# Optimization experiments

Measured on AMD Instinct MI355X. Metric: run time of the kernel, lower is better.

## Reference

```python
import jax, jax.numpy as jnp
import numpy as np

B, C, C2, E = 4, 1024, 1024, 1024
D = 1024          # context_size (d_q = d_kv)
NH = 16           # module's n_heads arg -> actual head_dim after the quirky view
G = D // NH       # effective number of head groups = 64


def setup_inputs() -> dict:
    key = jax.random.key(0)
    ks = jax.random.split(key, 6)
    s = 0.02
    return {
        "x1": jax.random.normal(ks[0], (B, C, E), dtype=jnp.float32),
        "x2": jax.random.normal(ks[1], (B, C2, E), dtype=jnp.float32),
        "W_q": jax.random.normal(ks[2], (E, D), dtype=jnp.float32) * s,
        "W_k": jax.random.normal(ks[3], (E, D), dtype=jnp.float32) * s,
        "W_v": jax.random.normal(ks[4], (E, D), dtype=jnp.float32) * s,
        "W_o": jax.random.normal(ks[5], (D, D), dtype=jnp.float32) * s,
    }


def _split_heads(t):
    # (B, S, D) -> view (B, S, G, NH) -> transpose(1,2) -> (B, G, S, NH)
    b, s, _ = t.shape
    return jnp.transpose(t.reshape(b, s, G, NH), (0, 2, 1, 3))


def reference(x1, x2, W_q, W_k, W_v, W_o):
    Q = _split_heads(x1 @ W_q)   # (B, G, C, NH)
    K = _split_heads(x2 @ W_k)   # (B, G, C2, NH)
    V = _split_heads(x2 @ W_v)   # (B, G, C2, NH)
    scale = 1.0 / jnp.sqrt(jnp.asarray(NH, dtype=Q.dtype))
    scores = jnp.einsum("bgqh,bgkh->bgqk", Q, K) * scale  # (B, G, C, C2)
    w = jax.nn.softmax(scores, axis=-1)
    out = jnp.einsum("bgqk,bgkh->bgqh", w, V)             # (B, G, C, NH)
    out = jnp.transpose(out, (0, 2, 1, 3)).reshape(B, C, D)
    return out @ W_o  # dropout p=0 -> identity
```

## Files before the change

### kernel.cpp

```cpp
#include <hip/hip_runtime.h>


typedef _Float16 f16x8 __attribute__((ext_vector_type(8)));
typedef _Float16 f16x4 __attribute__((ext_vector_type(4)));
typedef _Float16 f16x2 __attribute__((ext_vector_type(2)));
typedef float    f32x4 __attribute__((ext_vector_type(4)));

#define GLOAD_LDS16(gp, lp)                                              \
    __builtin_amdgcn_global_load_lds(                                    \
        (const __attribute__((address_space(1))) void*)(gp),             \
        (__attribute__((address_space(3))) void*)(lp), 16, 0, 0)

static __device__ __forceinline__ f16x8 pack8(f32x4 p0, f32x4 p1) {
    f16x2 a = __builtin_bit_cast(f16x2, __builtin_amdgcn_cvt_pkrtz(p0[0], p0[1]));
    f16x2 b = __builtin_bit_cast(f16x2, __builtin_amdgcn_cvt_pkrtz(p0[2], p0[3]));
    f16x2 c = __builtin_bit_cast(f16x2, __builtin_amdgcn_cvt_pkrtz(p1[0], p1[1]));
    f16x2 d = __builtin_bit_cast(f16x2, __builtin_amdgcn_cvt_pkrtz(p1[2], p1[3]));
    f16x8 r;
    r[0] = a[0]; r[1] = a[1]; r[2] = b[0]; r[3] = b[1];
    r[4] = c[0]; r[5] = c[1]; r[6] = d[0]; r[7] = d[1];
    return r;
}

__global__ __launch_bounds__(256) void cvt2_kernel(const float* __restrict__ x1,
                                                   const float* __restrict__ x2,
                                                   _Float16* __restrict__ y1,
                                                   _Float16* __restrict__ y2) {
    int i = blockIdx.x * 256 + threadIdx.x;
    const float* x = (i < 1048576) ? x1 : x2;
    _Float16* y = (i < 1048576) ? y1 : y2;
    int j = i & 1048575;
    float4 v = ((const float4*)x)[j];
    f16x4 h = { (_Float16)v.x, (_Float16)v.y, (_Float16)v.z, (_Float16)v.w };
    ((f16x4*)y)[j] = h;
}

__global__ __launch_bounds__(256) void transpose_cvt4_kernel(
        const float* __restrict__ W0, const float* __restrict__ W1,
        const float* __restrict__ W2, const float* __restrict__ W3,
        _Float16* __restrict__ T0, _Float16* __restrict__ T1,
        _Float16* __restrict__ T2, _Float16* __restrict__ T3) {
    int z = blockIdx.z;
    const float* W = (z == 0) ? W0 : (z == 1) ? W1 : (z == 2) ? W2 : W3;
    _Float16* WT = (z == 0) ? T0 : (z == 1) ? T1 : (z == 2) ? T2 : T3;
    __shared__ float tile[32][33];
    int tx = threadIdx.x, ty = threadIdx.y;
    int c0 = blockIdx.x * 32, r0 = blockIdx.y * 32;
#pragma unroll
    for (int i = 0; i < 32; i += 8)
        tile[ty + i][tx] = W[(r0 + ty + i) * 1024 + (c0 + tx)];
    __syncthreads();
#pragma unroll
    for (int i = 0; i < 32; i += 8)
        WT[(c0 + ty + i) * 1024 + (r0 + tx)] = (_Float16)tile[tx][ty + i];
}

template <bool OUTF32>
static __device__ __forceinline__ void gemm_body(const _Float16* __restrict__ A,
                                                 const _Float16* __restrict__ BT,
                                                 void* __restrict__ Cout,
                                                 _Float16* As, _Float16* Bs) {
    const int tid = threadIdx.x, lane = tid & 63, wave = tid >> 6;
    const int wm = wave >> 1, wn = wave & 1;
    const int col = lane & 15, quad = lane >> 4;
    const int m0 = blockIdx.y * 128, n0 = blockIdx.x * 128;

    f32x4 acc[4][4];
#pragma unroll
    for (int i = 0; i < 4; i++)
#pragma unroll
        for (int j = 0; j < 4; j++) acc[i][j] = (f32x4){0.f, 0.f, 0.f, 0.f};

    const int srow = wave * 8 + (lane >> 3);
    const int sch = (lane & 7) * 8;
    const _Float16* Ag = A + (size_t)(m0 + srow) * 1024 + sch;
    const _Float16* Bg = BT + (size_t)(n0 + srow) * 1024 + sch;
    _Float16* Asl = As + wave * 512;
    _Float16* Bsl = Bs + wave * 512;

    for (int kt = 0; kt < 16; kt++) {
        __syncthreads();
#pragma unroll
        for (int c = 0; c < 4; c++) {
            GLOAD_LDS16(Ag + (size_t)(c * 32) * 1024 + kt * 64, Asl + c * 2048);
            GLOAD_LDS16(Bg + (size_t)(c * 32) * 1024 + kt * 64, Bsl + c * 2048);
        }
        __syncthreads();
#pragma unroll
        for (int ki = 0; ki < 2; ki++) {
            f16x8 af[4], bf[4];
#pragma unroll
            for (int i = 0; i < 4; i++)
                af[i] = *(const f16x8*)(As + (wm * 64 + i * 16 + col) * 64 + ki * 32 + quad * 8);
#pragma unroll
            for (int j = 0; j < 4; j++)
                bf[j] = *(const f16x8*)(Bs + (wn * 64 + j * 16 + col) * 64 + ki * 32 + quad * 8);
#pragma unroll
            for (int i = 0; i < 4; i++)
#pragma unroll
                for (int j = 0; j < 4; j++)
                    acc[i][j] = __builtin_amdgcn_mfma_f32_16x16x32_f16(af[i], bf[j], acc[i][j], 0, 0, 0);
        }
    }

#pragma unroll
    for (int i = 0; i < 4; i++)
#pragma unroll
        for (int ii = 0; ii < 4; ii++) {
            int row = m0 + wm * 64 + i * 16 + quad * 4 + ii;
#pragma unroll
            for (int j = 0; j < 4; j++) {
                int cc = n0 + wn * 64 + j * 16 + col;
                if (OUTF32) ((float*)Cout)[(size_t)row * 1024 + cc] = acc[i][j][ii];
                else ((_Float16*)Cout)[(size_t)row * 1024 + cc] = (_Float16)acc[i][j][ii];
            }
        }
}

__global__ __launch_bounds__(256, 3) void gemm_qkv_kernel(
        const _Float16* __restrict__ x1h, const _Float16* __restrict__ x2h,
        const _Float16* __restrict__ WqT, const _Float16* __restrict__ WkT,
        const _Float16* __restrict__ WvT,
        _Float16* __restrict__ Qh, _Float16* __restrict__ Kh, _Float16* __restrict__ Vh) {
    __shared__ _Float16 As[128 * 64], Bs[128 * 64];
    int z = blockIdx.z;
    const _Float16* A = (z == 0) ? x1h : x2h;
    const _Float16* BT = (z == 0) ? WqT : (z == 1) ? WkT : WvT;
    _Float16* C = (z == 0) ? Qh : (z == 1) ? Kh : Vh;
    gemm_body<false>(A, BT, (void*)C, As, Bs);
}

__global__ __launch_bounds__(256, 3) void gemm_wo_kernel(const _Float16* __restrict__ Ah,
                                                         const _Float16* __restrict__ WoT,
                                                         float* __restrict__ out) {
    __shared__ _Float16 As[128 * 64], Bs[128 * 64];
    gemm_body<true>(Ah, WoT, (void*)out, As, Bs);
}

__global__ __launch_bounds__(512, 8) void attn_kernel(const _Float16* __restrict__ Qh,
                                                      const _Float16* __restrict__ Kh,
                                                      const _Float16* __restrict__ Vh,
                                                      _Float16* __restrict__ Ah) {
    int pair = blockIdx.y;
    int b = pair >> 6, g = pair & 63;
    __shared__ _Float16 Ks[512 * 16];
    __shared__ _Float16 Vts[16 * 512];

    const _Float16* Kg = Kh + (size_t)(b * 1024) * 1024 + g * 16;
    const _Float16* Vg = Vh + (size_t)(b * 1024) * 1024 + g * 16;
    int tid = threadIdx.x;
    int lane = tid & 63, wave = tid >> 6;
    int col = lane & 15, quad = lane >> 4;
    int q0 = blockIdx.x * 256 + wave * 32;

    f16x4 qf[2];
    const _Float16* qb = Qh + (size_t)(b * 1024 + q0 + col) * 1024 + g * 16 + quad * 4;
#pragma unroll
    for (int qg = 0; qg < 2; qg++) {
        f16x4 t = *(const f16x4*)(qb + (size_t)qg * 16 * 1024);
#pragma unroll
        for (int j = 0; j < 4; j++) qf[qg][j] = (_Float16)((float)t[j] * 0.360673760f);
    }

    f32x4 O[2], L[2];
#pragma unroll
    for (int qg = 0; qg < 2; qg++) {
        O[qg] = (f32x4){0.f, 0.f, 0.f, 0.f};
        L[qg] = (f32x4){0.f, 0.f, 0.f, 0.f};
    }
    f16x8 ones8;
#pragma unroll
    for (int j = 0; j < 8; j++) ones8[j] = (_Float16)1.f;
    const f32x4 zero = {0.f, 0.f, 0.f, 0.f};
    const int krow0 = (col >> 2) * 8 + (col & 3);
    const int vrot = 72 * col;

    for (int c = 0; c < 2; c++) {
        if (c) __syncthreads();
#pragma unroll
        for (int it = 0; it < 2; it++) {
            int row = it * 256 + (tid >> 1);
            int part = (tid & 1) * 8;
            *(uint4*)(Ks + row * 16 + part) =
                *(const uint4*)(Kg + (size_t)(c * 512 + row) * 1024 + part);
        }
#pragma unroll
        for (int it = 0; it < 2; it++) {
            int row = it * 256 + (tid >> 1);
            int part = (tid & 1) * 8;
            f16x8 v = *(const f16x8*)(Vg + (size_t)(c * 512 + row) * 1024 + part);
#pragma unroll
            for (int j = 0; j < 8; j++) {
                int h = part + j;
                Vts[h * 512 + ((row + 72 * h) & 511)] = v[j];
            }
        }
        __syncthreads();

#pragma unroll 4
        for (int t = 0; t < 16; t++) {
            const _Float16* kb = Ks + (t * 32 + krow0) * 16 + quad * 4;
            f16x4 ak0 = *(const f16x4*)(kb);
            f16x4 ak1 = *(const f16x4*)(kb + 4 * 16);
            f16x8 av = *(const f16x8*)(Vts + col * 512 + ((t * 32 + quad * 8 + vrot) & 511));
#pragma unroll
            for (int qg = 0; qg < 2; qg++) {
                f32x4 s0 = __builtin_amdgcn_mfma_f32_16x16x16f16(ak0, qf[qg], zero, 0, 0, 0);
                f32x4 s1 = __builtin_amdgcn_mfma_f32_16x16x16f16(ak1, qf[qg], zero, 0, 0, 0);
                f32x4 p0, p1;
#pragma unroll
                for (int i = 0; i < 4; i++) p0[i] = __builtin_amdgcn_exp2f(s0[i]);
#pragma unroll
                for (int i = 0; i < 4; i++) p1[i] = __builtin_amdgcn_exp2f(s1[i]);
                f16x8 pb = pack8(p0, p1);
                O[qg] = __builtin_amdgcn_mfma_f32_16x16x32_f16(av, pb, O[qg], 0, 0, 0);
                L[qg] = __builtin_amdgcn_mfma_f32_16x16x32_f16(ones8, pb, L[qg], 0, 0, 0);
            }
        }
    }

    _Float16* ob = Ah + (size_t)(b * 1024 + q0 + col) * 1024 + g * 16 + quad * 4;
#pragma unroll
    for (int qg = 0; qg < 2; qg++) {
        float rl = 1.0f / L[qg][0];
        f16x4 ov;
#pragma unroll
        for (int i = 0; i < 4; i++) ov[i] = (_Float16)(O[qg][i] * rl);
        *(f16x4*)(ob + (size_t)qg * 16 * 1024) = ov;
    }
}

extern "C" void kernel_launch(void* const* d_in, const int* in_sizes, int n_in,
                              void* d_out, int out_size, void* d_ws, size_t ws_size,
                              hipStream_t stream) {
    const float* x1 = (const float*)d_in[0];
    const float* x2 = (const float*)d_in[1];
    const float* Wq = (const float*)d_in[2];
    const float* Wk = (const float*)d_in[3];
    const float* Wv = (const float*)d_in[4];
    const float* Wo = (const float*)d_in[5];

    char* ws = (char*)d_ws;
    const size_t MB = 1u << 20;
    if (ws_size < 56 * MB) return;

    _Float16* x1h = (_Float16*)(ws + 0 * MB);
    _Float16* x2h = (_Float16*)(ws + 8 * MB);
    _Float16* WqT = (_Float16*)(ws + 16 * MB);
    _Float16* WkT = (_Float16*)(ws + 18 * MB);
    _Float16* WvT = (_Float16*)(ws + 20 * MB);
    _Float16* WoT = (_Float16*)(ws + 22 * MB);
    _Float16* Qh  = (_Float16*)(ws + 24 * MB);
    _Float16* Kh  = (_Float16*)(ws + 32 * MB);
    _Float16* Vh  = (_Float16*)(ws + 40 * MB);
    _Float16* Ah  = (_Float16*)(ws + 48 * MB);

    cvt2_kernel<<<8192, 256, 0, stream>>>(x1, x2, x1h, x2h);

    transpose_cvt4_kernel<<<dim3(32, 32, 4), dim3(32, 8), 0, stream>>>(
        Wq, Wk, Wv, Wo, WqT, WkT, WvT, WoT);

    gemm_qkv_kernel<<<dim3(8, 32, 3), 256, 0, stream>>>(x1h, x2h, WqT, WkT, WvT, Qh, Kh, Vh);

    attn_kernel<<<dim3(4, 256), 512, 0, stream>>>(Qh, Kh, Vh, Ah);

    gemm_wo_kernel<<<dim3(8, 32), 256, 0, stream>>>(Ah, WoT, (float*)d_out);
}
```

Before: 210.4 us.

## Switch attention to 32x32x16 MFMA with fused row-sum and merge prep kernels

The attention inner loop now uses 32x32x16 MFMA instructions for both the score and PV products. Lanes 16-31 of the B operand read a shared vector of ones, so the softmax denominator lands in the same accumulator and the separate L MFMA is gone. K and V are stored in shared memory with new permuted layouts that match the larger MFMA operand shapes. The input conversion and weight transpose kernels are also merged into one launch, removing one kernel's launch overhead. The risks are higher register pressure from the 16-wide accumulator and possible bank conflicts in the new LDS layouts.

```diff
diff --git a/kernel.cpp b/kernel.cpp
--- a/kernel.cpp
+++ b/kernel.cpp
@@ -5,54 +5,56 @@
 typedef _Float16 f16x4 __attribute__((ext_vector_type(4)));
 typedef _Float16 f16x2 __attribute__((ext_vector_type(2)));
 typedef float    f32x4 __attribute__((ext_vector_type(4)));
+typedef float    f32x16 __attribute__((ext_vector_type(16)));
 
 #define GLOAD_LDS16(gp, lp)                                              \
     __builtin_amdgcn_global_load_lds(                                    \
         (const __attribute__((address_space(1))) void*)(gp),             \
         (__attribute__((address_space(3))) void*)(lp), 16, 0, 0)
 
-static __device__ __forceinline__ f16x8 pack8(f32x4 p0, f32x4 p1) {
-    f16x2 a = __builtin_bit_cast(f16x2, __builtin_amdgcn_cvt_pkrtz(p0[0], p0[1]));
-    f16x2 b = __builtin_bit_cast(f16x2, __builtin_amdgcn_cvt_pkrtz(p0[2], p0[3]));
-    f16x2 c = __builtin_bit_cast(f16x2, __builtin_amdgcn_cvt_pkrtz(p1[0], p1[1]));
-    f16x2 d = __builtin_bit_cast(f16x2, __builtin_amdgcn_cvt_pkrtz(p1[2], p1[3]));
+static __device__ __forceinline__ f16x8 pack8f(const float* p) {
+    f16x2 a = __builtin_bit_cast(f16x2, __builtin_amdgcn_cvt_pkrtz(p[0], p[1]));
+    f16x2 b = __builtin_bit_cast(f16x2, __builtin_amdgcn_cvt_pkrtz(p[2], p[3]));
+    f16x2 c = __builtin_bit_cast(f16x2, __builtin_amdgcn_cvt_pkrtz(p[4], p[5]));
+    f16x2 d = __builtin_bit_cast(f16x2, __builtin_amdgcn_cvt_pkrtz(p[6], p[7]));
     f16x8 r;
     r[0] = a[0]; r[1] = a[1]; r[2] = b[0]; r[3] = b[1];
     r[4] = c[0]; r[5] = c[1]; r[6] = d[0]; r[7] = d[1];
     return r;
 }
 
-__global__ __launch_bounds__(256) void cvt2_kernel(const float* __restrict__ x1,
-                                                   const float* __restrict__ x2,
-                                                   _Float16* __restrict__ y1,
-                                                   _Float16* __restrict__ y2) {
-    int i = blockIdx.x * 256 + threadIdx.x;
-    const float* x = (i < 1048576) ? x1 : x2;
-    _Float16* y = (i < 1048576) ? y1 : y2;
-    int j = i & 1048575;
-    float4 v = ((const float4*)x)[j];
-    f16x4 h = { (_Float16)v.x, (_Float16)v.y, (_Float16)v.z, (_Float16)v.w };
-    ((f16x4*)y)[j] = h;
-}
-
-__global__ __launch_bounds__(256) void transpose_cvt4_kernel(
+__global__ __launch_bounds__(256) void prep_kernel(
+        const float* __restrict__ x1, const float* __restrict__ x2,
         const float* __restrict__ W0, const float* __restrict__ W1,
         const float* __restrict__ W2, const float* __restrict__ W3,
+        _Float16* __restrict__ y1, _Float16* __restrict__ y2,
         _Float16* __restrict__ T0, _Float16* __restrict__ T1,
         _Float16* __restrict__ T2, _Float16* __restrict__ T3) {
-    int z = blockIdx.z;
-    const float* W = (z == 0) ? W0 : (z == 1) ? W1 : (z == 2) ? W2 : W3;
-    _Float16* WT = (z == 0) ? T0 : (z == 1) ? T1 : (z == 2) ? T2 : T3;
-    __shared__ float tile[32][33];
-    int tx = threadIdx.x, ty = threadIdx.y;
-    int c0 = blockIdx.x * 32, r0 = blockIdx.y * 32;
-#pragma unroll
-    for (int i = 0; i < 32; i += 8)
-        tile[ty + i][tx] = W[(r0 + ty + i) * 1024 + (c0 + tx)];
-    __syncthreads();
-#pragma unroll
-    for (int i = 0; i < 32; i += 8)
-        WT[(c0 + ty + i) * 1024 + (r0 + tx)] = (_Float16)tile[tx][ty + i];
+    int bx = blockIdx.x, tid = threadIdx.x;
+    if (bx < 8192) {
+        int i = bx * 256 + tid;
+        const float* x = (i < 1048576) ? x1 : x2;
+        _Float16* y = (i < 1048576) ? y1 : y2;
+        int j = i & 1048575;
+        float4 v = ((const float4*)x)[j];
+        f16x4 h = { (_Float16)v.x, (_Float16)v.y, (_Float16)v.z, (_Float16)v.w };
+        ((f16x4*)y)[j] = h;
+    } else {
+        int z = (bx - 8192) >> 10;
+        const float* W = (z == 0) ? W0 : (z == 1) ? W1 : (z == 2) ? W2 : W3;
+        _Float16* WT = (z == 0) ? T0 : (z == 1) ? T1 : (z == 2) ? T2 : T3;
+        int t = (bx - 8192) & 1023;
+        int c0 = (t & 31) * 32, r0 = (t >> 5) * 32;
+        __shared__ float tile[32][33];
+        int tx = tid & 31, ty = tid >> 5;
+#pragma unroll
+        for (int i = 0; i < 32; i += 8)
+            tile[ty + i][tx] = W[(r0 + ty + i) * 1024 + (c0 + tx)];
+        __syncthreads();
+#pragma unroll
+        for (int i = 0; i < 32; i += 8)
+            WT[(c0 + ty + i) * 1024 + (r0 + tx)] = (_Float16)tile[tx][ty + i];
+    }
 }
 
 template <bool OUTF32>
@@ -143,91 +145,78 @@
                                                       _Float16* __restrict__ Ah) {
     int pair = blockIdx.y;
     int b = pair >> 6, g = pair & 63;
-    __shared__ _Float16 Ks[512 * 16];
-    __shared__ _Float16 Vts[16 * 512];
+    __shared__ _Float16 KA[8192];
+    __shared__ _Float16 VA[8192];
+    __shared__ _Float16 ones[8];
 
     const _Float16* Kg = Kh + (size_t)(b * 1024) * 1024 + g * 16;
     const _Float16* Vg = Vh + (size_t)(b * 1024) * 1024 + g * 16;
     int tid = threadIdx.x;
+    if (tid < 8) ones[tid] = (_Float16)1.f;
+
     int lane = tid & 63, wave = tid >> 6;
-    int col = lane & 15, quad = lane >> 4;
+    int n = lane & 31, h5 = lane >> 5;
     int q0 = blockIdx.x * 256 + wave * 32;
 
-    f16x4 qf[2];
-    const _Float16* qb = Qh + (size_t)(b * 1024 + q0 + col) * 1024 + g * 16 + quad * 4;
-#pragma unroll
-    for (int qg = 0; qg < 2; qg++) {
-        f16x4 t = *(const f16x4*)(qb + (size_t)qg * 16 * 1024);
-#pragma unroll
-        for (int j = 0; j < 4; j++) qf[qg][j] = (_Float16)((float)t[j] * 0.360673760f);
-    }
-
-    f32x4 O[2], L[2];
-#pragma unroll
-    for (int qg = 0; qg < 2; qg++) {
-        O[qg] = (f32x4){0.f, 0.f, 0.f, 0.f};
-        L[qg] = (f32x4){0.f, 0.f, 0.f, 0.f};
-    }
-    f16x8 ones8;
-#pragma unroll
-    for (int j = 0; j < 8; j++) ones8[j] = (_Float16)1.f;
-    const f32x4 zero = {0.f, 0.f, 0.f, 0.f};
-    const int krow0 = (col >> 2) * 8 + (col & 3);
-    const int vrot = 72 * col;
+    f16x8 qf;
+    {
+        f16x8 t = *(const f16x8*)(Qh + (size_t)(b * 1024 + q0 + n) * 1024 + g * 16 + h5 * 8);
+#pragma unroll
+        for (int j = 0; j < 8; j++) qf[j] = (_Float16)((float)t[j] * 0.360673760f);
+    }
+
+    f32x16 acc = {0.f, 0.f, 0.f, 0.f, 0.f, 0.f, 0.f, 0.f,
+                  0.f, 0.f, 0.f, 0.f, 0.f, 0.f, 0.f, 0.f};
+    const f32x16 zero16 = acc;
+    const _Float16* vbase = (n < 16) ? (VA + (n + 16 * h5) * 8) : ones;
+    const int vstep = (n < 16) ? 256 : 0;
 
     for (int c = 0; c < 2; c++) {
         if (c) __syncthreads();
 #pragma unroll
         for (int it = 0; it < 2; it++) {
             int row = it * 256 + (tid >> 1);
-            int part = (tid & 1) * 8;
-            *(uint4*)(Ks + row * 16 + part) =
-                *(const uint4*)(Kg + (size_t)(c * 512 + row) * 1024 + part);
+            int part = tid & 1;
+            int pm = (row & 19) | ((row & 4) << 1) | ((row & 8) >> 1);
+            *(uint4*)(KA + (((row >> 5) * 64) + pm + 32 * part) * 8) =
+                *(const uint4*)(Kg + (size_t)(c * 512 + row) * 1024 + part * 8);
         }
 #pragma unroll
         for (int it = 0; it < 2; it++) {
             int row = it * 256 + (tid >> 1);
-            int part = (tid & 1) * 8;
-            f16x8 v = *(const f16x8*)(Vg + (size_t)(c * 512 + row) * 1024 + part);
-#pragma unroll
-            for (int j = 0; j < 8; j++) {
-                int h = part + j;
-                Vts[h * 512 + ((row + 72 * h) & 511)] = v[j];
-            }
-        }
-        __syncthreads();
-
-#pragma unroll 4
+            int part = tid & 1;
+            f16x8 v = *(const f16x8*)(Vg + (size_t)(c * 512 + row) * 1024 + part * 8);
+            int base = (row >> 4) * 256 + ((row >> 3) & 1) * 128 + part * 64 + (row & 7);
+#pragma unroll
+            for (int j = 0; j < 8; j++) VA[base + j * 8] = v[j];
+        }
+        __syncthreads();
+
+#pragma unroll 2
         for (int t = 0; t < 16; t++) {
-            const _Float16* kb = Ks + (t * 32 + krow0) * 16 + quad * 4;
-            f16x4 ak0 = *(const f16x4*)(kb);
-            f16x4 ak1 = *(const f16x4*)(kb + 4 * 16);
-            f16x8 av = *(const f16x8*)(Vts + col * 512 + ((t * 32 + quad * 8 + vrot) & 511));
-#pragma unroll
-            for (int qg = 0; qg < 2; qg++) {
-                f32x4 s0 = __builtin_amdgcn_mfma_f32_16x16x16f16(ak0, qf[qg], zero, 0, 0, 0);
-                f32x4 s1 = __builtin_amdgcn_mfma_f32_16x16x16f16(ak1, qf[qg], zero, 0, 0, 0);
-                f32x4 p0, p1;
-#pragma unroll
-                for (int i = 0; i < 4; i++) p0[i] = __builtin_amdgcn_exp2f(s0[i]);
-#pragma unroll
-                for (int i = 0; i < 4; i++) p1[i] = __builtin_amdgcn_exp2f(s1[i]);
-                f16x8 pb = pack8(p0, p1);
-                O[qg] = __builtin_amdgcn_mfma_f32_16x16x32_f16(av, pb, O[qg], 0, 0, 0);
-                L[qg] = __builtin_amdgcn_mfma_f32_16x16x32_f16(ones8, pb, L[qg], 0, 0, 0);
-            }
-        }
-    }
-
-    _Float16* ob = Ah + (size_t)(b * 1024 + q0 + col) * 1024 + g * 16 + quad * 4;
-#pragma unroll
-    for (int qg = 0; qg < 2; qg++) {
-        float rl = 1.0f / L[qg][0];
-        f16x4 ov;
-#pragma unroll
-        for (int i = 0; i < 4; i++) ov[i] = (_Float16)(O[qg][i] * rl);
-        *(f16x4*)(ob + (size_t)qg * 16 * 1024) = ov;
-    }
+            f16x8 ak = *(const f16x8*)(KA + (t * 64 + lane) * 8);
+            f32x16 s = __builtin_amdgcn_mfma_f32_32x32x16_f16(ak, qf, zero16, 0, 0, 0);
+            float p[16];
+#pragma unroll
+            for (int i = 0; i < 16; i++) p[i] = __builtin_amdgcn_exp2f(s[i]);
+            f16x8 pb0 = pack8f(p);
+            f16x8 pb1 = pack8f(p + 8);
+            f16x8 av0 = *(const f16x8*)(vbase + (2 * t) * vstep);
+            f16x8 av1 = *(const f16x8*)(vbase + (2 * t + 1) * vstep);
+            acc = __builtin_amdgcn_mfma_f32_32x32x16_f16(av0, pb0, acc, 0, 0, 0);
+            acc = __builtin_amdgcn_mfma_f32_32x32x16_f16(av1, pb1, acc, 0, 0, 0);
+        }
+    }
+
+    float rl = 1.0f / acc[8];
+    f16x4 o0, o1;
+#pragma unroll
+    for (int i = 0; i < 4; i++) o0[i] = (_Float16)(acc[i] * rl);
+#pragma unroll
+    for (int i = 0; i < 4; i++) o1[i] = (_Float16)(acc[4 + i] * rl);
+    _Float16* ob = Ah + (size_t)(b * 1024 + q0 + n) * 1024 + g * 16 + h5 * 4;
+    *(f16x4*)(ob) = o0;
+    *(f16x4*)(ob + 8) = o1;
 }
 
 extern "C" void kernel_launch(void* const* d_in, const int* in_sizes, int n_in,
@@ -255,10 +244,8 @@
     _Float16* Vh  = (_Float16*)(ws + 40 * MB);
     _Float16* Ah  = (_Float16*)(ws + 48 * MB);
 
-    cvt2_kernel<<<8192, 256, 0, stream>>>(x1, x2, x1h, x2h);
-
-    transpose_cvt4_kernel<<<dim3(32, 32, 4), dim3(32, 8), 0, stream>>>(
-        Wq, Wk, Wv, Wo, WqT, WkT, WvT, WoT);
+    prep_kernel<<<12288, 256, 0, stream>>>(x1, x2, Wq, Wk, Wv, Wo,
+                                           x1h, x2h, WqT, WkT, WvT, WoT);
 
     gemm_qkv_kernel<<<dim3(8, 32, 3), 256, 0, stream>>>(x1h, x2h, WqT, WkT, WvT, Qh, Kh, Vh);
 
```

After: 197.9 us. 6.0% less time.
